# Performance work log

Hardware: AMD Instinct MI355X
Metric: run time of the kernel (lower is better)

The kernel has to match this reference:

```python
import jax, jax.numpy as jnp
import numpy as np

N = 50000
NFEAT = 256
NHID = 64
NHEADS = 8
E_RAND = 1600000
ALPHA = 0.2  # leaky relu negative slope


def setup_inputs() -> dict:
    key = jax.random.key(0)
    kx, ke1, ke2, kw, ka, kwo, kao = jax.random.split(key, 7)
    x = jax.random.normal(kx, (N, NFEAT), dtype=jnp.float32)
    src = jax.random.randint(ke1, (E_RAND,), 0, N)
    dst = jax.random.randint(ke2, (E_RAND,), 0, N)
    loops = jnp.arange(N)
    edge_index = jnp.stack([jnp.concatenate([src, loops]),
                            jnp.concatenate([dst, loops])], axis=0)  # [2, 1650000]
    # learned params (xavier-ish scale)
    W = jax.random.normal(kw, (NHEADS, NFEAT, NHID), dtype=jnp.float32) * (1.0 / np.sqrt(NFEAT))
    a = jax.random.normal(ka, (NHEADS, 2 * NHID), dtype=jnp.float32) * (1.0 / np.sqrt(2 * NHID))
    W_out = jax.random.normal(kwo, (NHID * NHEADS, 1), dtype=jnp.float32) * (1.0 / np.sqrt(NHID * NHEADS))
    a_out = jax.random.normal(kao, (2,), dtype=jnp.float32) * (1.0 / np.sqrt(2.0))
    return {"x": x, "edge_index": edge_index, "W": W, "a": a,
            "W_out": W_out, "a_out": a_out}


def _sp_gat_layer(x, edge_index, W_l, a_l, concat):
    """pyGAT SpGraphAttentionLayer forward (eval mode: dropout = identity)."""
    src, dst = edge_index[0], edge_index[1]
    h = x @ W_l                              # [N, F']
    F_ = h.shape[1]
    # a^T [h_src || h_dst] = (a1.h)[src] + (a2.h)[dst] -- avoids [2F', E] concat
    f1 = h @ a_l[:F_]                        # [N]
    f2 = h @ a_l[F_:]                        # [N]
    s = f1[src] + f2[dst]                    # [E]
    e = jnp.exp(-jax.nn.leaky_relu(s, ALPHA))  # [E], note the minus sign (pyGAT)
    rowsum = jax.ops.segment_sum(e, src, num_segments=N)          # [N]
    num = jax.ops.segment_sum(e[:, None] * h[dst], src, num_segments=N)  # [N, F']
    out = num / rowsum[:, None]
    return jax.nn.elu(out) if concat else out


def reference(x, edge_index, W, a, W_out, a_out):
    # input dropout is identity in eval mode
    heads = [_sp_gat_layer(x, edge_index, W[i], a[i], concat=True)
             for i in range(NHEADS)]
    h = jnp.concatenate(heads, axis=1)       # [N, NHEADS*NHID]
    out = _sp_gat_layer(h, edge_index, W_out, a_out, concat=False)  # [N, 1]
    return jax.nn.sigmoid(jax.nn.elu(out))
```

## Files before the change

kernel.cpp:

```cpp
#include <hip/hip_runtime.h>
#include <hip/hip_bf16.h>
#include <hip/hip_fp16.h>
#include <math.h>

#define N_NODES 50000
#define NFEAT 256
#define NHID 64
#define NHEADS 8
#define FTOT 512
#define E_TOT 1650000
#define ALPHA 0.2f
#define NB_SCAN 196
#define ALDS 264

typedef short s16x4 __attribute__((ext_vector_type(4)));
typedef short s16x8 __attribute__((ext_vector_type(8)));
typedef float f32x4 __attribute__((ext_vector_type(4)));
typedef float f32x2 __attribute__((ext_vector_type(2)));

__device__ __forceinline__ short f2bf(float f) {
  unsigned u = __float_as_uint(f);
  unsigned r = u + 0x7fffu + ((u >> 16) & 1u);
  return (short)(r >> 16);
}

__device__ __forceinline__ unsigned char f2fp8(float f) {
  return (unsigned char)(__builtin_amdgcn_cvt_pk_fp8_f32(f, 0.f, 0, false) & 0xff);
}

__device__ __forceinline__ float att_e(float f1v, float g) {
  float s = f1v + g;
  float lk = (s > 0.f) ? s : ALPHA * s;
  return expf(-lk);
}

__device__ __forceinline__ void fma8_fp8(float e, uint2 u, float* acc) {
  f32x2 p;
  p = __builtin_amdgcn_cvt_pk_f32_fp8(u.x, false);
  acc[0] += e * p[0]; acc[1] += e * p[1];
  p = __builtin_amdgcn_cvt_pk_f32_fp8(u.x, true);
  acc[2] += e * p[0]; acc[3] += e * p[1];
  p = __builtin_amdgcn_cvt_pk_f32_fp8(u.y, false);
  acc[4] += e * p[0]; acc[5] += e * p[1];
  p = __builtin_amdgcn_cvt_pk_f32_fp8(u.y, true);
  acc[6] += e * p[0]; acc[7] += e * p[1];
}

__global__ __launch_bounds__(256) void setup_kernel(
    const float* __restrict__ W, short* __restrict__ Wt,
    const int* __restrict__ src, int* __restrict__ cnt,
    int* __restrict__ rank) {
  int b = blockIdx.x, t = threadIdx.x;
  if (b < 512) {
    int idx = b * 256 + t;
    int h = idx >> 14, r = idx & 16383, k = r >> 6, j = r & 63;
    Wt[h * 16384 + j * 256 + k] = f2bf(W[idx]);
  } else {
    int i = (b - 512) * 256 + t;
    if (i < E_TOT) rank[i] = atomicAdd(&cnt[src[i]], 1);
  }
}

__global__ __launch_bounds__(512) void gemm_mfma_kernel(
    const float* __restrict__ x, const short* __restrict__ Wt,
    const float* __restrict__ a, unsigned char* __restrict__ h1,
    float* __restrict__ f1, float* __restrict__ f2) {
  __shared__ __align__(16) short A_s[64 * ALDS];
  int bm = blockIdx.x * 64;
  int t = threadIdx.x;
  int wid = t >> 6, l = t & 63;
  int lr = l & 15, lk = l >> 4;
  int arow = t >> 3, acol = (t & 7) * 4;
  const short* wbase = Wt + wid * 16384 + lr * 256 + lk * 8;
  int gr = bm + arow;
  float4 xr[8];
#pragma unroll
  for (int i = 0; i < 8; ++i) {
    if (gr < N_NODES)
      xr[i] = *reinterpret_cast<const float4*>(x + (size_t)gr * NFEAT + i * 32 + acol);
    else
      xr[i] = make_float4(0.f, 0.f, 0.f, 0.f);
  }
#pragma unroll
  for (int i = 0; i < 8; ++i) {
    s16x4 v;
    v[0] = f2bf(xr[i].x); v[1] = f2bf(xr[i].y);
    v[2] = f2bf(xr[i].z); v[3] = f2bf(xr[i].w);
    *reinterpret_cast<s16x4*>(&A_s[arow * ALDS + i * 32 + acol]) = v;
  }
  __syncthreads();
  f32x4 acc[4][4] = {};
  for (int k0 = 0; k0 < NFEAT; k0 += 32) {
    s16x8 bf[4];
#pragma unroll
    for (int nj = 0; nj < 4; ++nj)
      bf[nj] = *reinterpret_cast<const s16x8*>(wbase + nj * 16 * 256 + k0);
    s16x8 af[4];
#pragma unroll
    for (int mi = 0; mi < 4; ++mi)
      af[mi] = *reinterpret_cast<const s16x8*>(
          &A_s[(mi * 16 + lr) * ALDS + k0 + lk * 8]);
#pragma unroll
    for (int mi = 0; mi < 4; ++mi)
#pragma unroll
      for (int nj = 0; nj < 4; ++nj)
        acc[mi][nj] = __builtin_amdgcn_mfma_f32_16x16x32_bf16(
            af[mi], bf[nj], acc[mi][nj], 0, 0, 0);
  }
#pragma unroll
  for (int mi = 0; mi < 4; ++mi) {
#pragma unroll
    for (int nj = 0; nj < 4; ++nj) {
#pragma unroll
      for (int q = 0; q < 4; ++q) {
        int r = bm + mi * 16 + lk * 4 + q;
        if (r < N_NODES)
          h1[(size_t)r * FTOT + wid * 64 + nj * 16 + lr] = f2fp8(acc[mi][nj][q]);
      }
    }
  }
  float a1v[4], a2v[4];
#pragma unroll
  for (int nj = 0; nj < 4; ++nj) {
    a1v[nj] = a[wid * 128 + nj * 16 + lr];
    a2v[nj] = a[wid * 128 + 64 + nj * 16 + lr];
  }
#pragma unroll
  for (int mi = 0; mi < 4; ++mi) {
#pragma unroll
    for (int q = 0; q < 4; ++q) {
      float p1 = 0.f, p2 = 0.f;
#pragma unroll
      for (int nj = 0; nj < 4; ++nj) {
        p1 += acc[mi][nj][q] * a1v[nj];
        p2 += acc[mi][nj][q] * a2v[nj];
      }
      p1 += __shfl_xor(p1, 1); p2 += __shfl_xor(p2, 1);
      p1 += __shfl_xor(p1, 2); p2 += __shfl_xor(p2, 2);
      p1 += __shfl_xor(p1, 4); p2 += __shfl_xor(p2, 4);
      p1 += __shfl_xor(p1, 8); p2 += __shfl_xor(p2, 8);
      int r = bm + mi * 16 + lk * 4 + q;
      if (lr == 0 && r < N_NODES) {
        f1[r * 8 + wid] = p1;
        f2[r * 8 + wid] = p2;
      }
    }
  }
}

__global__ __launch_bounds__(256) void scan1_kernel(const int* __restrict__ cnt,
                                                    int* __restrict__ offs,
                                                    int* __restrict__ bsum) {
  __shared__ int sh[256];
  int b = blockIdx.x, t = threadIdx.x, i = b * 256 + t;
  int v = (i < N_NODES) ? cnt[i] : 0;
  sh[t] = v;
  __syncthreads();
  for (int o = 1; o < 256; o <<= 1) {
    int u = (t >= o) ? sh[t - o] : 0;
    __syncthreads();
    sh[t] += u;
    __syncthreads();
  }
  if (i < N_NODES) offs[i] = sh[t] - v;
  if (t == 255) bsum[b] = sh[255];
}

__global__ __launch_bounds__(256) void scan2_kernel(int* __restrict__ bsum,
                                                    int* __restrict__ offs) {
  __shared__ int sh[256];
  int t = threadIdx.x;
  int v = (t < NB_SCAN) ? bsum[t] : 0;
  sh[t] = v;
  __syncthreads();
  for (int o = 1; o < 256; o <<= 1) {
    int u = (t >= o) ? sh[t - o] : 0;
    __syncthreads();
    sh[t] += u;
    __syncthreads();
  }
  if (t < NB_SCAN) bsum[t] = sh[t] - v;
  if (t == 255) offs[N_NODES] = sh[255];
}

__global__ __launch_bounds__(256) void scan3_kernel(int* __restrict__ offs,
                                                    const int* __restrict__ bsum) {
  int i = blockIdx.x * 256 + threadIdx.x;
  if (i < N_NODES) offs[i] += bsum[blockIdx.x];
}

__global__ __launch_bounds__(256) void scatter_kernel(
    const int* __restrict__ src, const int* __restrict__ dst,
    const int* __restrict__ offsets, const int* __restrict__ rank,
    int* __restrict__ edst) {
  int i = blockIdx.x * 256 + threadIdx.x;
  if (i < E_TOT) {
    int s = src[i];
    edst[offsets[s] + rank[i]] = dst[i];
  }
}

__global__ __launch_bounds__(256) void aggregate_kernel(
    const unsigned char* __restrict__ h1, const float* __restrict__ f1,
    const float* __restrict__ f2, const int* __restrict__ offsets,
    const int* __restrict__ edst, const float* __restrict__ W_out,
    float* __restrict__ hout) {
  int n = blockIdx.x * 4 + (threadIdx.x >> 6);
  int l = threadIdx.x & 63;
  int head = l >> 3;
  int beg = offsets[n], end = offsets[n + 1];
  float f1v = f1[n * 8 + head];
  float4 w0 = *reinterpret_cast<const float4*>(W_out + l * 8);
  float4 w1 = *reinterpret_cast<const float4*>(W_out + l * 8 + 4);
  float acc[8] = {};
  float rs = 0.f;
  int j = beg;
  for (; j + 3 < end; j += 4) {
    int d0 = edst[j], d1 = edst[j + 1], d2 = edst[j + 2], d3 = edst[j + 3];
    uint2 u0 = *reinterpret_cast<const uint2*>(h1 + (size_t)d0 * FTOT + l * 8);
    uint2 u1 = *reinterpret_cast<const uint2*>(h1 + (size_t)d1 * FTOT + l * 8);
    uint2 u2 = *reinterpret_cast<const uint2*>(h1 + (size_t)d2 * FTOT + l * 8);
    uint2 u3 = *reinterpret_cast<const uint2*>(h1 + (size_t)d3 * FTOT + l * 8);
    float g0 = f2[d0 * 8 + head];
    float g1 = f2[d1 * 8 + head];
    float g2 = f2[d2 * 8 + head];
    float g3 = f2[d3 * 8 + head];
    float e0 = att_e(f1v, g0), e1 = att_e(f1v, g1);
    float e2 = att_e(f1v, g2), e3 = att_e(f1v, g3);
    rs += (e0 + e1) + (e2 + e3);
    fma8_fp8(e0, u0, acc);
    fma8_fp8(e1, u1, acc);
    fma8_fp8(e2, u2, acc);
    fma8_fp8(e3, u3, acc);
  }
  for (; j < end; ++j) {
    int d = edst[j];
    uint2 u = *reinterpret_cast<const uint2*>(h1 + (size_t)d * FTOT + l * 8);
    float e = att_e(f1v, f2[d * 8 + head]);
    rs += e;
    fma8_fp8(e, u, acc);
  }
  float inv = 1.f / rs;
  float v = 0.f;
  const float* wp0 = reinterpret_cast<const float*>(&w0);
  const float* wp1 = reinterpret_cast<const float*>(&w1);
#pragma unroll
  for (int k = 0; k < 8; ++k) {
    float o = acc[k] * inv;
    o = (o > 0.f) ? o : expm1f(o);
    float wk = (k < 4) ? wp0[k] : wp1[k - 4];
    v += o * wk;
  }
#pragma unroll
  for (int o = 32; o > 0; o >>= 1) v += __shfl_down(v, o);
  if (l == 0) hout[n] = v;
}

__global__ __launch_bounds__(256) void layer2_kernel(
    const int* __restrict__ offsets, const int* __restrict__ edst,
    const float* __restrict__ hout, const float* __restrict__ a_out,
    float* __restrict__ out) {
  int n = blockIdx.x * 4 + (threadIdx.x >> 6);
  int l = threadIdx.x & 63;
  float a0 = a_out[0], a1 = a_out[1];
  int beg = offsets[n], end = offsets[n + 1];
  float f1v = hout[n] * a0;
  float rs = 0.f, num = 0.f;
  for (int j = beg + l; j < end; j += 64) {
    int d = edst[j];
    float hd = hout[d];
    float s = f1v + a1 * hd;
    float lk = (s > 0.f) ? s : ALPHA * s;
    float e = expf(-lk);
    rs += e;
    num += e * hd;
  }
#pragma unroll
  for (int o = 32; o > 0; o >>= 1) {
    rs += __shfl_down(rs, o);
    num += __shfl_down(num, o);
  }
  if (l == 0) {
    float o_ = num / rs;
    float el = (o_ > 0.f) ? o_ : expm1f(o_);
    out[n] = 1.f / (1.f + expf(-el));
  }
}

extern "C" void kernel_launch(void* const* d_in, const int* in_sizes, int n_in,
                              void* d_out, int out_size, void* d_ws, size_t ws_size,
                              hipStream_t stream) {
  const float* x = (const float*)d_in[0];
  const int* ei = (const int*)d_in[1];
  const float* W = (const float*)d_in[2];
  const float* a = (const float*)d_in[3];
  const float* W_out = (const float*)d_in[4];
  const float* a_out = (const float*)d_in[5];
  float* out = (float*)d_out;
  const int* src = ei;
  const int* dst = ei + E_TOT;

  char* p = (char*)d_ws;
  auto carve = [&](size_t bytes) {
    char* r = p;
    p += (bytes + 255) & ~(size_t)255;
    return r;
  };
  unsigned char* h1 = (unsigned char*)carve((size_t)N_NODES * FTOT);
  float* f1 = (float*)carve((size_t)N_NODES * 8 * 4);
  float* f2 = (float*)carve((size_t)N_NODES * 8 * 4);
  int* offsets = (int*)carve((size_t)(N_NODES + 1) * 4);
  int* cnt = (int*)carve((size_t)N_NODES * 4);
  int* rank = (int*)carve((size_t)E_TOT * 4);
  int* edst = (int*)carve((size_t)E_TOT * 4);
  int* bsum = (int*)carve((size_t)NB_SCAN * 4);
  short* Wt = (short*)carve((size_t)NHEADS * NFEAT * NHID * 2);
  float* hout = (float*)carve((size_t)N_NODES * 4);

  hipMemsetAsync(cnt, 0, (size_t)N_NODES * 4, stream);

  setup_kernel<<<512 + 6446, 256, 0, stream>>>(W, Wt, src, cnt, rank);
  gemm_mfma_kernel<<<782, 512, 0, stream>>>(x, Wt, a, h1, f1, f2);
  scan1_kernel<<<NB_SCAN, 256, 0, stream>>>(cnt, offsets, bsum);
  scan2_kernel<<<1, 256, 0, stream>>>(bsum, offsets);
  scan3_kernel<<<NB_SCAN, 256, 0, stream>>>(offsets, bsum);
  scatter_kernel<<<6446, 256, 0, stream>>>(src, dst, offsets, rank, edst);
  aggregate_kernel<<<12500, 256, 0, stream>>>(h1, f1, f2, offsets, edst, W_out, hout);
  layer2_kernel<<<12500, 256, 0, stream>>>(offsets, edst, hout, a_out, out);
}
```

Measured before the change: 316.9 us.

## Fuse GEMM with edge scatter, use packed FMA and fast exp2

Moves the scans ahead of the GEMM and merges the GEMM and CSR scatter into one launch, so the scatter blocks run alongside the GEMM blocks and one kernel launch is saved. The aggregation now accumulates with packed two-wide float vectors, and the leaky-relu exponentials use fmax plus the hardware exp2 builtin instead of expf. Wave index is made scalar with readfirstlane. Risks: the fused kernel's scatter blocks reserve 512-thread slots and the LDS declared for the GEMM path, and exp2 is slightly less accurate than expf.

```diff
diff --git a/kernel.cpp b/kernel.cpp
--- a/kernel.cpp
+++ b/kernel.cpp
@@ -12,6 +12,9 @@
 #define ALPHA 0.2f
 #define NB_SCAN 196
 #define ALDS 264
+#define GEMM_BLKS 782
+#define SCAT_BLKS 3223
+#define LOG2E 1.442695040888963f
 
 typedef short s16x4 __attribute__((ext_vector_type(4)));
 typedef short s16x8 __attribute__((ext_vector_type(8)));
@@ -30,20 +33,16 @@
 
 __device__ __forceinline__ float att_e(float f1v, float g) {
   float s = f1v + g;
-  float lk = (s > 0.f) ? s : ALPHA * s;
-  return expf(-lk);
-}
-
-__device__ __forceinline__ void fma8_fp8(float e, uint2 u, float* acc) {
-  f32x2 p;
-  p = __builtin_amdgcn_cvt_pk_f32_fp8(u.x, false);
-  acc[0] += e * p[0]; acc[1] += e * p[1];
-  p = __builtin_amdgcn_cvt_pk_f32_fp8(u.x, true);
-  acc[2] += e * p[0]; acc[3] += e * p[1];
-  p = __builtin_amdgcn_cvt_pk_f32_fp8(u.y, false);
-  acc[4] += e * p[0]; acc[5] += e * p[1];
-  p = __builtin_amdgcn_cvt_pk_f32_fp8(u.y, true);
-  acc[6] += e * p[0]; acc[7] += e * p[1];
+  float lk = fmaxf(s, ALPHA * s);
+  return __builtin_amdgcn_exp2f(-LOG2E * lk);
+}
+
+__device__ __forceinline__ void fma8_fp8(float e, uint2 u, f32x2* acc2) {
+  f32x2 ev; ev[0] = e; ev[1] = e;
+  acc2[0] += ev * __builtin_amdgcn_cvt_pk_f32_fp8(u.x, false);
+  acc2[1] += ev * __builtin_amdgcn_cvt_pk_f32_fp8(u.x, true);
+  acc2[2] += ev * __builtin_amdgcn_cvt_pk_f32_fp8(u.y, false);
+  acc2[3] += ev * __builtin_amdgcn_cvt_pk_f32_fp8(u.y, true);
 }
 
 __global__ __launch_bounds__(256) void setup_kernel(
@@ -61,10 +60,59 @@
   }
 }
 
-__global__ __launch_bounds__(512) void gemm_mfma_kernel(
+__global__ __launch_bounds__(256) void scan1_kernel(const int* __restrict__ cnt,
+                                                    int* __restrict__ offs,
+                                                    int* __restrict__ bsum) {
+  __shared__ int sh[256];
+  int b = blockIdx.x, t = threadIdx.x, i = b * 256 + t;
+  int v = (i < N_NODES) ? cnt[i] : 0;
+  sh[t] = v;
+  __syncthreads();
+  for (int o = 1; o < 256; o <<= 1) {
+    int u = (t >= o) ? sh[t - o] : 0;
+    __syncthreads();
+    sh[t] += u;
+    __syncthreads();
+  }
+  if (i < N_NODES) offs[i] = sh[t] - v;
+  if (t == 255) bsum[b] = sh[255];
+}
+
+__global__ __launch_bounds__(256) void scan2_kernel(int* __restrict__ bsum,
+                                                    int* __restrict__ offs) {
+  __shared__ int sh[256];
+  int t = threadIdx.x;
+  int v = (t < NB_SCAN) ? bsum[t] : 0;
+  sh[t] = v;
+  __syncthreads();
+  for (int o = 1; o < 256; o <<= 1) {
+    int u = (t >= o) ? sh[t - o] : 0;
+    __syncthreads();
+    sh[t] += u;
+    __syncthreads();
+  }
+  if (t < NB_SCAN) bsum[t] = sh[t] - v;
+  if (t == 255) offs[N_NODES] = sh[255];
+}
+
+__global__ __launch_bounds__(256) void scan3_kernel(int* __restrict__ offs,
+                                                    const int* __restrict__ bsum) {
+  int i = blockIdx.x * 256 + threadIdx.x;
+  if (i < N_NODES) offs[i] += bsum[blockIdx.x];
+}
+
+__global__ __launch_bounds__(512) void gemm_scatter_kernel(
     const float* __restrict__ x, const short* __restrict__ Wt,
     const float* __restrict__ a, unsigned char* __restrict__ h1,
-    float* __restrict__ f1, float* __restrict__ f2) {
+    float* __restrict__ f1, float* __restrict__ f2,
+    const int* __restrict__ src, const int* __restrict__ dst,
+    const int* __restrict__ offsets, const int* __restrict__ rank,
+    int* __restrict__ edst) {
+  if (blockIdx.x >= GEMM_BLKS) {
+    int i = (blockIdx.x - GEMM_BLKS) * 512 + threadIdx.x;
+    if (i < E_TOT) edst[offsets[src[i]] + rank[i]] = dst[i];
+    return;
+  }
   __shared__ __align__(16) short A_s[64 * ALDS];
   int bm = blockIdx.x * 64;
   int t = threadIdx.x;
@@ -148,71 +196,18 @@
   }
 }
 
-__global__ __launch_bounds__(256) void scan1_kernel(const int* __restrict__ cnt,
-                                                    int* __restrict__ offs,
-                                                    int* __restrict__ bsum) {
-  __shared__ int sh[256];
-  int b = blockIdx.x, t = threadIdx.x, i = b * 256 + t;
-  int v = (i < N_NODES) ? cnt[i] : 0;
-  sh[t] = v;
-  __syncthreads();
-  for (int o = 1; o < 256; o <<= 1) {
-    int u = (t >= o) ? sh[t - o] : 0;
-    __syncthreads();
-    sh[t] += u;
-    __syncthreads();
-  }
-  if (i < N_NODES) offs[i] = sh[t] - v;
-  if (t == 255) bsum[b] = sh[255];
-}
-
-__global__ __launch_bounds__(256) void scan2_kernel(int* __restrict__ bsum,
-                                                    int* __restrict__ offs) {
-  __shared__ int sh[256];
-  int t = threadIdx.x;
-  int v = (t < NB_SCAN) ? bsum[t] : 0;
-  sh[t] = v;
-  __syncthreads();
-  for (int o = 1; o < 256; o <<= 1) {
-    int u = (t >= o) ? sh[t - o] : 0;
-    __syncthreads();
-    sh[t] += u;
-    __syncthreads();
-  }
-  if (t < NB_SCAN) bsum[t] = sh[t] - v;
-  if (t == 255) offs[N_NODES] = sh[255];
-}
-
-__global__ __launch_bounds__(256) void scan3_kernel(int* __restrict__ offs,
-                                                    const int* __restrict__ bsum) {
-  int i = blockIdx.x * 256 + threadIdx.x;
-  if (i < N_NODES) offs[i] += bsum[blockIdx.x];
-}
-
-__global__ __launch_bounds__(256) void scatter_kernel(
-    const int* __restrict__ src, const int* __restrict__ dst,
-    const int* __restrict__ offsets, const int* __restrict__ rank,
-    int* __restrict__ edst) {
-  int i = blockIdx.x * 256 + threadIdx.x;
-  if (i < E_TOT) {
-    int s = src[i];
-    edst[offsets[s] + rank[i]] = dst[i];
-  }
-}
-
 __global__ __launch_bounds__(256) void aggregate_kernel(
     const unsigned char* __restrict__ h1, const float* __restrict__ f1,
     const float* __restrict__ f2, const int* __restrict__ offsets,
     const int* __restrict__ edst, const float* __restrict__ W_out,
     float* __restrict__ hout) {
-  int n = blockIdx.x * 4 + (threadIdx.x >> 6);
+  int wv = __builtin_amdgcn_readfirstlane(threadIdx.x >> 6);
+  int n = blockIdx.x * 4 + wv;
   int l = threadIdx.x & 63;
   int head = l >> 3;
   int beg = offsets[n], end = offsets[n + 1];
   float f1v = f1[n * 8 + head];
-  float4 w0 = *reinterpret_cast<const float4*>(W_out + l * 8);
-  float4 w1 = *reinterpret_cast<const float4*>(W_out + l * 8 + 4);
-  float acc[8] = {};
+  f32x2 acc2[4] = {};
   float rs = 0.f;
   int j = beg;
   for (; j + 3 < end; j += 4) {
@@ -228,28 +223,29 @@
     float e0 = att_e(f1v, g0), e1 = att_e(f1v, g1);
     float e2 = att_e(f1v, g2), e3 = att_e(f1v, g3);
     rs += (e0 + e1) + (e2 + e3);
-    fma8_fp8(e0, u0, acc);
-    fma8_fp8(e1, u1, acc);
-    fma8_fp8(e2, u2, acc);
-    fma8_fp8(e3, u3, acc);
+    fma8_fp8(e0, u0, acc2);
+    fma8_fp8(e1, u1, acc2);
+    fma8_fp8(e2, u2, acc2);
+    fma8_fp8(e3, u3, acc2);
   }
   for (; j < end; ++j) {
     int d = edst[j];
     uint2 u = *reinterpret_cast<const uint2*>(h1 + (size_t)d * FTOT + l * 8);
     float e = att_e(f1v, f2[d * 8 + head]);
     rs += e;
-    fma8_fp8(e, u, acc);
+    fma8_fp8(e, u, acc2);
   }
   float inv = 1.f / rs;
   float v = 0.f;
-  const float* wp0 = reinterpret_cast<const float*>(&w0);
-  const float* wp1 = reinterpret_cast<const float*>(&w1);
-#pragma unroll
-  for (int k = 0; k < 8; ++k) {
-    float o = acc[k] * inv;
-    o = (o > 0.f) ? o : expm1f(o);
-    float wk = (k < 4) ? wp0[k] : wp1[k - 4];
-    v += o * wk;
+  const float* wop = W_out + l * 8;
+#pragma unroll
+  for (int k = 0; k < 4; ++k) {
+#pragma unroll
+    for (int q = 0; q < 2; ++q) {
+      float o = acc2[k][q] * inv;
+      o = (o > 0.f) ? o : expm1f(o);
+      v += o * wop[k * 2 + q];
+    }
   }
 #pragma unroll
   for (int o = 32; o > 0; o >>= 1) v += __shfl_down(v, o);
@@ -260,7 +256,8 @@
     const int* __restrict__ offsets, const int* __restrict__ edst,
     const float* __restrict__ hout, const float* __restrict__ a_out,
     float* __restrict__ out) {
-  int n = blockIdx.x * 4 + (threadIdx.x >> 6);
+  int wv = __builtin_amdgcn_readfirstlane(threadIdx.x >> 6);
+  int n = blockIdx.x * 4 + wv;
   int l = threadIdx.x & 63;
   float a0 = a_out[0], a1 = a_out[1];
   int beg = offsets[n], end = offsets[n + 1];
@@ -270,8 +267,8 @@
     int d = edst[j];
     float hd = hout[d];
     float s = f1v + a1 * hd;
-    float lk = (s > 0.f) ? s : ALPHA * s;
-    float e = expf(-lk);
+    float lk = fmaxf(s, ALPHA * s);
+    float e = __builtin_amdgcn_exp2f(-LOG2E * lk);
     rs += e;
     num += e * hd;
   }
@@ -283,7 +280,7 @@
   if (l == 0) {
     float o_ = num / rs;
     float el = (o_ > 0.f) ? o_ : expm1f(o_);
-    out[n] = 1.f / (1.f + expf(-el));
+    out[n] = 1.f / (1.f + __builtin_amdgcn_exp2f(-LOG2E * el));
   }
 }
 
@@ -320,11 +317,11 @@
   hipMemsetAsync(cnt, 0, (size_t)N_NODES * 4, stream);
 
   setup_kernel<<<512 + 6446, 256, 0, stream>>>(W, Wt, src, cnt, rank);
-  gemm_mfma_kernel<<<782, 512, 0, stream>>>(x, Wt, a, h1, f1, f2);
   scan1_kernel<<<NB_SCAN, 256, 0, stream>>>(cnt, offsets, bsum);
   scan2_kernel<<<1, 256, 0, stream>>>(bsum, offsets);
   scan3_kernel<<<NB_SCAN, 256, 0, stream>>>(offsets, bsum);
-  scatter_kernel<<<6446, 256, 0, stream>>>(src, dst, offsets, rank, edst);
+  gemm_scatter_kernel<<<GEMM_BLKS + SCAT_BLKS, 512, 0, stream>>>(
+      x, Wt, a, h1, f1, f2, src, dst, offsets, rank, edst);
   aggregate_kernel<<<12500, 256, 0, stream>>>(h1, f1, f2, offsets, edst, W_out, hout);
   layer2_kernel<<<12500, 256, 0, stream>>>(offsets, edst, hout, a_out, out);
 }
```

Measured after the change: 291.7 us. 8.0% less time.
